# Kernel tuning notes

Measured on AMD Instinct MI355X. Metric: run time of the kernel, lower is better.

The kernel has to match this reference:

```python
import jax, jax.numpy as jnp
import numpy as np

B, N, C = 4, 2048, 768
H = 12
D = C // H  # head_dim = 64


def setup_inputs() -> dict:
    key = jax.random.key(0)
    k1, k2, k3, k4, k5 = jax.random.split(key, 5)
    s = 0.02
    return {
        "x": jax.random.normal(k1, (B, N, C), dtype=jnp.float32),
        "qkv_w": jax.random.normal(k2, (3 * C, C), dtype=jnp.float32) * s,
        "qkv_b": jax.random.normal(k3, (3 * C,), dtype=jnp.float32) * s,
        "proj_w": jax.random.normal(k4, (C, C), dtype=jnp.float32) * s,
        "proj_b": jax.random.normal(k5, (C,), dtype=jnp.float32) * s,
    }


def reference(x, qkv_w, qkv_b, proj_w, proj_b):
    b, n, c = x.shape
    # qkv projection (torch Linear: x @ W.T + b) -> [B,N,3,H,D] -> [3,B,H,N,D]
    qkv = (x @ qkv_w.T + qkv_b).reshape(b, n, 3, H, D).transpose(2, 0, 3, 1, 4)
    q, k, v = qkv[0], qkv[1], qkv[2]
    scale = D ** (-0.5)
    attn = jnp.einsum("bhqd,bhkd->bhqk", q, k) * scale
    attn = jax.nn.softmax(attn, axis=-1)
    # dropout is identity in eval mode
    out = jnp.einsum("bhqk,bhkd->bhqd", attn, v)  # [B,H,N,D]
    out = out.transpose(0, 2, 1, 3).reshape(b, n, c)
    return out @ proj_w.T + proj_b
```

## Files before the change

### kernel.cpp

```cpp
#include <hip/hip_runtime.h>
#include <hip/hip_bf16.h>
#include <stdint.h>

typedef __bf16 bf16_t;
typedef __bf16 bf16x8 __attribute__((ext_vector_type(8)));
typedef float f32x4 __attribute__((ext_vector_type(4)));

#define NB 4
#define NH 12
#define ND 64
#define NN 2048
#define NC 768

__device__ __forceinline__ void async_copy16(const bf16_t* g, bf16_t* l) {
    __builtin_amdgcn_global_load_lds((__attribute__((address_space(1))) void*)(void*)g,
                                     (__attribute__((address_space(3))) void*)l, 16, 0, 0);
}

__global__ void cast_kernel(const float* __restrict__ src, bf16_t* __restrict__ dst, int n4) {
    int i = blockIdx.x * blockDim.x + threadIdx.x;
    if (i >= n4) return;
    float4 v = ((const float4*)src)[i];
    union { bf16_t e[4]; uint2 u; } t;
    t.e[0] = (bf16_t)v.x; t.e[1] = (bf16_t)v.y; t.e[2] = (bf16_t)v.z; t.e[3] = (bf16_t)v.w;
    ((uint2*)dst)[i] = t.u;
}

__device__ __forceinline__ int vperm(int s) {
    return (s & 32) | (((s >> 2) & 3) << 3) | (((s >> 4) & 1) << 2) | (s & 3);
}


__launch_bounds__(256)
__global__ void qkv_gemm_kernel(const bf16_t* __restrict__ X, const bf16_t* __restrict__ W,
                                const float* __restrict__ bias,
                                bf16_t* __restrict__ Q, bf16_t* __restrict__ K, bf16_t* __restrict__ V)
{
    __shared__ __align__(16) bf16_t sA[128 * 64];
    __shared__ __align__(16) bf16_t sB[128 * 64];
    const int tid  = threadIdx.x;
    const int lane = tid & 63;
    const int w    = tid >> 6;
    const int wm   = w & 1, wn = w >> 1;
    const int m0   = blockIdx.x * 128;
    const int n0   = blockIdx.y * 128;
    const int lrow = lane & 15;
    const int quad = lane >> 4;
    const int arow = lane >> 3;
    const int gch  = (lane & 7) ^ arow;

    const int colbase = n0 + wn * 64;
    const int t3 = colbase / NC;
    const int h  = (colbase % NC) / ND;

    f32x4 zero = {0.f, 0.f, 0.f, 0.f};
    f32x4 acc[4][4];
#pragma unroll
    for (int i = 0; i < 4; ++i)
#pragma unroll
        for (int j = 0; j < 4; ++j) acc[i][j] = zero;

    for (int kt = 0; kt < NC; kt += 64) {
        __syncthreads();
        for (int c = w; c < 16; c += 4) {
            async_copy16(X + (size_t)(m0 + c * 8 + arow) * NC + kt + gch * 8, sA + c * 512);
            async_copy16(W + (size_t)(n0 + c * 8 + arow) * NC + kt + gch * 8, sB + c * 512);
        }
        __syncthreads();
#pragma unroll
        for (int hh = 0; hh < 2; ++hh) {
            bf16x8 xf[4], wf[4];
#pragma unroll
            for (int i = 0; i < 4; ++i) {
                int r = wm * 64 + i * 16 + lrow;
                xf[i] = *(const bf16x8*)(sA + r * 64 + (((hh * 4 + quad) ^ (r & 7)) * 8));
            }
#pragma unroll
            for (int j = 0; j < 4; ++j) {
                int r = wn * 64 + j * 16 + lrow;
                wf[j] = *(const bf16x8*)(sB + r * 64 + (((hh * 4 + quad) ^ (r & 7)) * 8));
            }
            if (t3 < 2) {
#pragma unroll
                for (int i = 0; i < 4; ++i)
#pragma unroll
                    for (int j = 0; j < 4; ++j)
                        acc[i][j] = __builtin_amdgcn_mfma_f32_16x16x32_bf16(wf[j], xf[i], acc[i][j], 0, 0, 0);
            } else {
#pragma unroll
                for (int i = 0; i < 4; ++i)
#pragma unroll
                    for (int j = 0; j < 4; ++j)
                        acc[i][j] = __builtin_amdgcn_mfma_f32_16x16x32_bf16(xf[i], wf[j], acc[i][j], 0, 0, 0);
            }
        }
    }

    const float qscale = 0.125f * 1.44269504088896340736f;

    if (t3 < 2) {
        bf16_t* outb = t3 ? K : Q;
#pragma unroll
        for (int j = 0; j < 4; ++j) {
            const int dcol = j * 16 + quad * 4;
            const float4 bv4 = *(const float4*)(bias + colbase + dcol);
#pragma unroll
            for (int i = 0; i < 4; ++i) {
                const int tok = m0 + wm * 64 + i * 16 + lrow;
                const int bb = tok >> 11;
                const int nn = tok & 2047;
                union { bf16_t e[4]; uint2 u; } pk;
#pragma unroll
                for (int p = 0; p < 4; ++p) {
                    float val = acc[i][j][p] + (&bv4.x)[p];
                    if (t3 == 0) val *= qscale;
                    pk.e[p] = (bf16_t)val;
                }
                *(uint2*)(outb + ((size_t)(bb * NH + h) * NN + nn) * ND + dcol) = pk.u;
            }
        }
    } else {
#pragma unroll
        for (int j = 0; j < 4; ++j) {
            const int d  = j * 16 + lrow;
            const float bv = bias[colbase + d];
#pragma unroll
            for (int i = 0; i < 4; ++i) {
                const int tok0 = m0 + wm * 64 + i * 16 + quad * 4;
                const int bb = tok0 >> 11;
                const int nn = tok0 & 2047;
                union { bf16_t e[4]; uint2 u; } pk;
#pragma unroll
                for (int p = 0; p < 4; ++p) pk.e[p] = (bf16_t)(acc[i][j][p] + bv);
                const int pos = (nn & ~63) | vperm(nn & 63);
                *(uint2*)(V + ((size_t)(bb * NH + h) * ND + d) * NN + pos) = pk.u;
            }
        }
    }
}

__launch_bounds__(512)
__global__ void attn_kernel(const bf16_t* __restrict__ Q, const bf16_t* __restrict__ K,
                            const bf16_t* __restrict__ Vt, bf16_t* __restrict__ O)
{
    __shared__ __align__(16) bf16_t sQ[128 * 64];
    __shared__ __align__(16) bf16_t sK[2][64 * 64];
    __shared__ __align__(16) bf16_t sV[2][64 * 64];
    const int tid  = threadIdx.x;
    const int lane = tid & 63;
    const int w    = tid >> 6;
    const int qt   = blockIdx.x;
    const int h    = blockIdx.y;
    const int b    = blockIdx.z;
    const int lrow = lane & 15;
    const int quad = lane >> 4;
    const int arow = lane >> 3;
    const int gch  = (lane & 7) ^ arow;
    const size_t head_off = (size_t)(b * NH + h) * NN * ND;
    const bf16_t* qh = Q  + head_off;
    const bf16_t* kh = K  + head_off;
    const bf16_t* vh = Vt + head_off;

    for (int c = w; c < 16; c += 8)
        async_copy16(qh + (size_t)(qt * 128 + c * 8 + arow) * ND + gch * 8, sQ + c * 512);
    __syncthreads();

    bf16x8 qb[2];
#pragma unroll
    for (int hh = 0; hh < 2; ++hh)
        qb[hh] = *(const bf16x8*)(sQ + (w * 16 + lrow) * 64 + (((hh * 4 + quad) ^ (lrow & 7)) * 8));

    f32x4 zero = {0.f, 0.f, 0.f, 0.f};
    f32x4 o[4];
#pragma unroll
    for (int db = 0; db < 4; ++db) o[db] = zero;
    float l_i = 0.f;

    const bf16_t* kbase = kh + (size_t)(w * 8 + arow) * ND + gch * 8;
    const bf16_t* vbase = vh + (size_t)(w * 8 + arow) * NN + gch * 8;

    for (int it = 0; it < NN / 128; ++it) {
        __syncthreads();
        async_copy16(kbase + (size_t)(it * 128) * ND,      sK[0] + w * 512);
        async_copy16(kbase + (size_t)(it * 128 + 64) * ND, sK[1] + w * 512);
        async_copy16(vbase + it * 128,                     sV[0] + w * 512);
        async_copy16(vbase + it * 128 + 64,                sV[1] + w * 512);
        __syncthreads();

#pragma unroll
        for (int half = 0; half < 2; ++half) {
            const bf16_t* sKh = sK[half];
            const bf16_t* sVh = sV[half];
            f32x4 s[4];
#pragma unroll
            for (int blk = 0; blk < 4; ++blk) {
                int r = blk * 16 + lrow;
                bf16x8 a0 = *(const bf16x8*)(sKh + r * 64 + ((quad ^ (r & 7)) * 8));
                bf16x8 a1 = *(const bf16x8*)(sKh + r * 64 + (((4 + quad) ^ (r & 7)) * 8));
                f32x4 z = zero;
                z = __builtin_amdgcn_mfma_f32_16x16x32_bf16(a0, qb[0], z, 0, 0, 0);
                z = __builtin_amdgcn_mfma_f32_16x16x32_bf16(a1, qb[1], z, 0, 0, 0);
                s[blk] = z;
            }

            union { __hip_bfloat162 h2[8]; bf16x8 v[2]; } pe;
            float rs0 = 0.f, rs1 = 0.f;
#pragma unroll
            for (int blk = 0; blk < 4; ++blk) {
                float e0 = exp2f(s[blk][0]);
                float e1 = exp2f(s[blk][1]);
                float e2 = exp2f(s[blk][2]);
                float e3 = exp2f(s[blk][3]);
                rs0 += e0 + e1;
                rs1 += e2 + e3;
                const int hb = (blk >> 1) * 4 + (blk & 1) * 2;
                pe.h2[hb]     = __float22bfloat162_rn(make_float2(e0, e1));
                pe.h2[hb + 1] = __float22bfloat162_rn(make_float2(e2, e3));
            }
            l_i += rs0 + rs1;

#pragma unroll
            for (int db = 0; db < 4; ++db) {
                int r = db * 16 + lrow;
                bf16x8 v0 = *(const bf16x8*)(sVh + r * 64 + ((quad ^ (r & 7)) * 8));
                bf16x8 v1 = *(const bf16x8*)(sVh + r * 64 + (((4 + quad) ^ (r & 7)) * 8));
                o[db] = __builtin_amdgcn_mfma_f32_16x16x32_bf16(v0, pe.v[0], o[db], 0, 0, 0);
                o[db] = __builtin_amdgcn_mfma_f32_16x16x32_bf16(v1, pe.v[1], o[db], 0, 0, 0);
            }
        }
    }

    l_i += __shfl_xor(l_i, 16);
    l_i += __shfl_xor(l_i, 32);
    const float rl = 1.0f / l_i;

    const int n = qt * 128 + w * 16 + lrow;
    const size_t rowoff = ((size_t)(b * NN + n)) * NC + h * ND;
#pragma unroll
    for (int db = 0; db < 4; ++db) {
        union { bf16_t e[4]; uint2 u; } pk;
#pragma unroll
        for (int p = 0; p < 4; ++p) pk.e[p] = (bf16_t)(o[db][p] * rl);
        *(uint2*)(O + rowoff + db * 16 + quad * 4) = pk.u;
    }
}

__launch_bounds__(256)
__global__ void proj_gemm_kernel(const bf16_t* __restrict__ A, const bf16_t* __restrict__ W,
                                 const float* __restrict__ bias, float* __restrict__ out)
{
    __shared__ __align__(16) bf16_t sA[128 * 64];
    __shared__ __align__(16) bf16_t sB[128 * 64];
    const int tid  = threadIdx.x;
    const int lane = tid & 63;
    const int w    = tid >> 6;
    const int wm   = w & 1, wn = w >> 1;
    const int m0   = blockIdx.x * 128;
    const int n0   = blockIdx.y * 128;
    const int lrow = lane & 15;
    const int quad = lane >> 4;
    const int arow = lane >> 3;
    const int gch  = (lane & 7) ^ arow;

    f32x4 zero = {0.f, 0.f, 0.f, 0.f};
    f32x4 acc[4][4];
#pragma unroll
    for (int i = 0; i < 4; ++i)
#pragma unroll
        for (int j = 0; j < 4; ++j) acc[i][j] = zero;

    for (int kt = 0; kt < NC; kt += 64) {
        __syncthreads();
        for (int c = w; c < 16; c += 4) {
            async_copy16(A + (size_t)(m0 + c * 8 + arow) * NC + kt + gch * 8, sA + c * 512);
            async_copy16(W + (size_t)(n0 + c * 8 + arow) * NC + kt + gch * 8, sB + c * 512);
        }
        __syncthreads();
#pragma unroll
        for (int hh = 0; hh < 2; ++hh) {
            bf16x8 xf[4], wf[4];
#pragma unroll
            for (int i = 0; i < 4; ++i) {
                int r = wm * 64 + i * 16 + lrow;
                xf[i] = *(const bf16x8*)(sA + r * 64 + (((hh * 4 + quad) ^ (r & 7)) * 8));
            }
#pragma unroll
            for (int j = 0; j < 4; ++j) {
                int r = wn * 64 + j * 16 + lrow;
                wf[j] = *(const bf16x8*)(sB + r * 64 + (((hh * 4 + quad) ^ (r & 7)) * 8));
            }
#pragma unroll
            for (int i = 0; i < 4; ++i)
#pragma unroll
                for (int j = 0; j < 4; ++j)
                    acc[i][j] = __builtin_amdgcn_mfma_f32_16x16x32_bf16(wf[j], xf[i], acc[i][j], 0, 0, 0);
        }
    }

#pragma unroll
    for (int j = 0; j < 4; ++j) {
        const int colg0 = n0 + wn * 64 + j * 16 + quad * 4;
        const float4 bv4 = *(const float4*)(bias + colg0);
#pragma unroll
        for (int i = 0; i < 4; ++i) {
            const int tok = m0 + wm * 64 + i * 16 + lrow;
            float4 val;
#pragma unroll
            for (int p = 0; p < 4; ++p) (&val.x)[p] = acc[i][j][p] + (&bv4.x)[p];
            *(float4*)(out + (size_t)tok * NC + colg0) = val;
        }
    }
}

extern "C" void kernel_launch(void* const* d_in, const int* in_sizes, int n_in,
                              void* d_out, int out_size, void* d_ws, size_t ws_size,
                              hipStream_t stream) {
    const float* x      = (const float*)d_in[0];
    const float* qkv_w  = (const float*)d_in[1];
    const float* qkv_b  = (const float*)d_in[2];
    const float* proj_w = (const float*)d_in[3];
    const float* proj_b = (const float*)d_in[4];
    float* out = (float*)d_out;

    char* ws = (char*)d_ws;
    bf16_t* xb    = (bf16_t*)ws; ws += (size_t)8192 * 768 * 2;
    bf16_t* wqkv  = (bf16_t*)ws; ws += (size_t)2304 * 768 * 2;
    bf16_t* wproj = (bf16_t*)ws; ws += (size_t)768 * 768 * 2;
    bf16_t* qb    = (bf16_t*)ws; ws += (size_t)NB * NH * NN * ND * 2;
    bf16_t* kb    = (bf16_t*)ws; ws += (size_t)NB * NH * NN * ND * 2;
    bf16_t* vb    = (bf16_t*)ws; ws += (size_t)NB * NH * NN * ND * 2;
    bf16_t* ab    = (bf16_t*)ws; ws += (size_t)8192 * 768 * 2;

    cast_kernel<<<(8192 * 768 / 4 + 255) / 256, 256, 0, stream>>>(x, xb, 8192 * 768 / 4);
    cast_kernel<<<(2304 * 768 / 4 + 255) / 256, 256, 0, stream>>>(qkv_w, wqkv, 2304 * 768 / 4);
    cast_kernel<<<(768 * 768 / 4 + 255) / 256, 256, 0, stream>>>(proj_w, wproj, 768 * 768 / 4);

    qkv_gemm_kernel<<<dim3(8192 / 128, 2304 / 128), 256, 0, stream>>>(xb, wqkv, qkv_b, qb, kb, vb);
    attn_kernel<<<dim3(NN / 128, NH, NB), 512, 0, stream>>>(qb, kb, vb, ab);
    proj_gemm_kernel<<<dim3(8192 / 128, 768 / 128), 256, 0, stream>>>(ab, wproj, proj_b, out);
}
```

Measured before the change: 234.9 us.

## Give each attention wave two query tiles, shrink blocks, split QKV GEMM by V

The attention kernel now runs 256 threads per block, and each wave handles 32 query rows (two 16-row tiles). Each K/V fragment read from LDS therefore feeds twice as many MFMAs. The Q, K and V buffers share one LDS array, and swizzle offsets are precomputed. The QKV GEMM is split into two template launches (Q/K and V) to remove a runtime branch around the MFMA loop. The trade-off is higher register pressure from the doubled accumulators, plus an extra kernel launch.

```diff
diff --git a/kernel.cpp b/kernel.cpp
--- a/kernel.cpp
+++ b/kernel.cpp
@@ -5,6 +5,7 @@
 typedef __bf16 bf16_t;
 typedef __bf16 bf16x8 __attribute__((ext_vector_type(8)));
 typedef float f32x4 __attribute__((ext_vector_type(4)));
+typedef unsigned int u32x4 __attribute__((ext_vector_type(4)));
 
 #define NB 4
 #define NH 12
@@ -15,6 +16,13 @@
 __device__ __forceinline__ void async_copy16(const bf16_t* g, bf16_t* l) {
     __builtin_amdgcn_global_load_lds((__attribute__((address_space(1))) void*)(void*)g,
                                      (__attribute__((address_space(3))) void*)l, 16, 0, 0);
+}
+
+__device__ __forceinline__ unsigned pack_bf2(float a, float b) {
+    union { bf16_t e[2]; unsigned u; } t;
+    t.e[0] = (bf16_t)a;
+    t.e[1] = (bf16_t)b;
+    return t.u;
 }
 
 __global__ void cast_kernel(const float* __restrict__ src, bf16_t* __restrict__ dst, int n4) {
@@ -31,10 +39,12 @@
 }
 
 
+template <bool ISV>
 __launch_bounds__(256)
 __global__ void qkv_gemm_kernel(const bf16_t* __restrict__ X, const bf16_t* __restrict__ W,
                                 const float* __restrict__ bias,
-                                bf16_t* __restrict__ Q, bf16_t* __restrict__ K, bf16_t* __restrict__ V)
+                                bf16_t* __restrict__ Q, bf16_t* __restrict__ K, bf16_t* __restrict__ V,
+                                int n0base)
 {
     __shared__ __align__(16) bf16_t sA[128 * 64];
     __shared__ __align__(16) bf16_t sB[128 * 64];
@@ -43,15 +53,13 @@
     const int w    = tid >> 6;
     const int wm   = w & 1, wn = w >> 1;
     const int m0   = blockIdx.x * 128;
-    const int n0   = blockIdx.y * 128;
+    const int n0   = n0base + blockIdx.y * 128;
     const int lrow = lane & 15;
     const int quad = lane >> 4;
     const int arow = lane >> 3;
     const int gch  = (lane & 7) ^ arow;
 
     const int colbase = n0 + wn * 64;
-    const int t3 = colbase / NC;
-    const int h  = (colbase % NC) / ND;
 
     f32x4 zero = {0.f, 0.f, 0.f, 0.f};
     f32x4 acc[4][4];
@@ -80,25 +88,23 @@
                 int r = wn * 64 + j * 16 + lrow;
                 wf[j] = *(const bf16x8*)(sB + r * 64 + (((hh * 4 + quad) ^ (r & 7)) * 8));
             }
-            if (t3 < 2) {
-#pragma unroll
-                for (int i = 0; i < 4; ++i)
-#pragma unroll
-                    for (int j = 0; j < 4; ++j)
+#pragma unroll
+            for (int i = 0; i < 4; ++i)
+#pragma unroll
+                for (int j = 0; j < 4; ++j) {
+                    if (ISV)
+                        acc[i][j] = __builtin_amdgcn_mfma_f32_16x16x32_bf16(xf[i], wf[j], acc[i][j], 0, 0, 0);
+                    else
                         acc[i][j] = __builtin_amdgcn_mfma_f32_16x16x32_bf16(wf[j], xf[i], acc[i][j], 0, 0, 0);
-            } else {
-#pragma unroll
-                for (int i = 0; i < 4; ++i)
-#pragma unroll
-                    for (int j = 0; j < 4; ++j)
-                        acc[i][j] = __builtin_amdgcn_mfma_f32_16x16x32_bf16(xf[i], wf[j], acc[i][j], 0, 0, 0);
-            }
+                }
         }
     }
 
     const float qscale = 0.125f * 1.44269504088896340736f;
 
-    if (t3 < 2) {
+    if (!ISV) {
+        const int t3 = colbase / NC;
+        const int h  = (colbase % NC) / ND;
         bf16_t* outb = t3 ? K : Q;
 #pragma unroll
         for (int j = 0; j < 4; ++j) {
@@ -120,6 +126,7 @@
             }
         }
     } else {
+        const int h = (colbase - 2 * NC) / ND;
 #pragma unroll
         for (int j = 0; j < 4; ++j) {
             const int d  = j * 16 + lrow;
@@ -139,13 +146,12 @@
     }
 }
 
-__launch_bounds__(512)
+__launch_bounds__(256, 4)
 __global__ void attn_kernel(const bf16_t* __restrict__ Q, const bf16_t* __restrict__ K,
                             const bf16_t* __restrict__ Vt, bf16_t* __restrict__ O)
 {
-    __shared__ __align__(16) bf16_t sQ[128 * 64];
-    __shared__ __align__(16) bf16_t sK[2][64 * 64];
-    __shared__ __align__(16) bf16_t sV[2][64 * 64];
+    __shared__ __align__(16) bf16_t sKV[4][64 * 64];
+    bf16_t* sQ = sKV[0];
     const int tid  = threadIdx.x;
     const int lane = tid & 63;
     const int w    = tid >> 6;
@@ -161,87 +167,125 @@
     const bf16_t* kh = K  + head_off;
     const bf16_t* vh = Vt + head_off;
 
-    for (int c = w; c < 16; c += 8)
-        async_copy16(qh + (size_t)(qt * 128 + c * 8 + arow) * ND + gch * 8, sQ + c * 512);
+#pragma unroll
+    for (int c = 0; c < 4; ++c)
+        async_copy16(qh + (size_t)(qt * 128 + (w * 4 + c) * 8 + arow) * ND + gch * 8,
+                     sQ + (w * 4 + c) * 512);
     __syncthreads();
 
-    bf16x8 qb[2];
-#pragma unroll
-    for (int hh = 0; hh < 2; ++hh)
-        qb[hh] = *(const bf16x8*)(sQ + (w * 16 + lrow) * 64 + (((hh * 4 + quad) ^ (lrow & 7)) * 8));
+    bf16x8 qb[2][2];
+#pragma unroll
+    for (int qi = 0; qi < 2; ++qi)
+#pragma unroll
+        for (int hh = 0; hh < 2; ++hh) {
+            int r = w * 32 + qi * 16 + lrow;
+            qb[qi][hh] = *(const bf16x8*)(sQ + r * 64 + (((hh * 4 + quad) ^ (r & 7)) * 8));
+        }
+
+    int off[4][2];
+#pragma unroll
+    for (int blk = 0; blk < 4; ++blk) {
+        int r = blk * 16 + lrow;
+        off[blk][0] = r * 64 + ((quad ^ (r & 7)) * 8);
+        off[blk][1] = r * 64 + (((4 + quad) ^ (r & 7)) * 8);
+    }
 
     f32x4 zero = {0.f, 0.f, 0.f, 0.f};
-    f32x4 o[4];
-#pragma unroll
-    for (int db = 0; db < 4; ++db) o[db] = zero;
-    float l_i = 0.f;
-
-    const bf16_t* kbase = kh + (size_t)(w * 8 + arow) * ND + gch * 8;
-    const bf16_t* vbase = vh + (size_t)(w * 8 + arow) * NN + gch * 8;
+    f32x4 o[2][4];
+#pragma unroll
+    for (int qi = 0; qi < 2; ++qi)
+#pragma unroll
+        for (int db = 0; db < 4; ++db) o[qi][db] = zero;
+    float l_i[2] = {0.f, 0.f};
+
+    const bf16_t* kp = kh + (size_t)(w * 16 + arow) * ND + gch * 8;
+    const bf16_t* vp = vh + (size_t)(w * 16 + arow) * NN + gch * 8;
 
     for (int it = 0; it < NN / 128; ++it) {
         __syncthreads();
-        async_copy16(kbase + (size_t)(it * 128) * ND,      sK[0] + w * 512);
-        async_copy16(kbase + (size_t)(it * 128 + 64) * ND, sK[1] + w * 512);
-        async_copy16(vbase + it * 128,                     sV[0] + w * 512);
-        async_copy16(vbase + it * 128 + 64,                sV[1] + w * 512);
-        __syncthreads();
+        async_copy16(kp,               sKV[0] + w * 1024);
+        async_copy16(kp + 8 * ND,      sKV[0] + w * 1024 + 512);
+        async_copy16(kp + 64 * ND,     sKV[1] + w * 1024);
+        async_copy16(kp + 72 * ND,     sKV[1] + w * 1024 + 512);
+        async_copy16(vp,               sKV[2] + w * 1024);
+        async_copy16(vp + 8 * NN,      sKV[2] + w * 1024 + 512);
+        async_copy16(vp + 64,          sKV[3] + w * 1024);
+        async_copy16(vp + 8 * NN + 64, sKV[3] + w * 1024 + 512);
+        __syncthreads();
+        kp += 128 * ND;
+        vp += 128;
 
 #pragma unroll
         for (int half = 0; half < 2; ++half) {
-            const bf16_t* sKh = sK[half];
-            const bf16_t* sVh = sV[half];
-            f32x4 s[4];
+            const bf16_t* sKh = sKV[half];
+            const bf16_t* sVh = sKV[2 + half];
+
+            f32x4 s[2][4];
 #pragma unroll
             for (int blk = 0; blk < 4; ++blk) {
-                int r = blk * 16 + lrow;
-                bf16x8 a0 = *(const bf16x8*)(sKh + r * 64 + ((quad ^ (r & 7)) * 8));
-                bf16x8 a1 = *(const bf16x8*)(sKh + r * 64 + (((4 + quad) ^ (r & 7)) * 8));
-                f32x4 z = zero;
-                z = __builtin_amdgcn_mfma_f32_16x16x32_bf16(a0, qb[0], z, 0, 0, 0);
-                z = __builtin_amdgcn_mfma_f32_16x16x32_bf16(a1, qb[1], z, 0, 0, 0);
-                s[blk] = z;
-            }
-
-            union { __hip_bfloat162 h2[8]; bf16x8 v[2]; } pe;
-            float rs0 = 0.f, rs1 = 0.f;
-#pragma unroll
-            for (int blk = 0; blk < 4; ++blk) {
-                float e0 = exp2f(s[blk][0]);
-                float e1 = exp2f(s[blk][1]);
-                float e2 = exp2f(s[blk][2]);
-                float e3 = exp2f(s[blk][3]);
-                rs0 += e0 + e1;
-                rs1 += e2 + e3;
-                const int hb = (blk >> 1) * 4 + (blk & 1) * 2;
-                pe.h2[hb]     = __float22bfloat162_rn(make_float2(e0, e1));
-                pe.h2[hb + 1] = __float22bfloat162_rn(make_float2(e2, e3));
-            }
-            l_i += rs0 + rs1;
+                bf16x8 a0 = *(const bf16x8*)(sKh + off[blk][0]);
+                bf16x8 a1 = *(const bf16x8*)(sKh + off[blk][1]);
+#pragma unroll
+                for (int qi = 0; qi < 2; ++qi) {
+                    f32x4 z = zero;
+                    z = __builtin_amdgcn_mfma_f32_16x16x32_bf16(a0, qb[qi][0], z, 0, 0, 0);
+                    z = __builtin_amdgcn_mfma_f32_16x16x32_bf16(a1, qb[qi][1], z, 0, 0, 0);
+                    s[qi][blk] = z;
+                }
+            }
+
+            bf16x8 pe[2][2];
+#pragma unroll
+            for (int qi = 0; qi < 2; ++qi) {
+                u32x4 pu0 = {0, 0, 0, 0}, pu1 = {0, 0, 0, 0};
+                float r0 = 0.f, r1 = 0.f;
+#pragma unroll
+                for (int blk = 0; blk < 4; ++blk) {
+                    float e0 = __builtin_amdgcn_exp2f(s[qi][blk][0]);
+                    float e1 = __builtin_amdgcn_exp2f(s[qi][blk][1]);
+                    float e2 = __builtin_amdgcn_exp2f(s[qi][blk][2]);
+                    float e3 = __builtin_amdgcn_exp2f(s[qi][blk][3]);
+                    r0 += e0 + e1;
+                    r1 += e2 + e3;
+                    unsigned lo = pack_bf2(e0, e1), hi = pack_bf2(e2, e3);
+                    if (blk == 0)      { pu0[0] = lo; pu0[1] = hi; }
+                    else if (blk == 1) { pu0[2] = lo; pu0[3] = hi; }
+                    else if (blk == 2) { pu1[0] = lo; pu1[1] = hi; }
+                    else               { pu1[2] = lo; pu1[3] = hi; }
+                }
+                pe[qi][0] = __builtin_bit_cast(bf16x8, pu0);
+                pe[qi][1] = __builtin_bit_cast(bf16x8, pu1);
+                l_i[qi] += r0 + r1;
+            }
 
 #pragma unroll
             for (int db = 0; db < 4; ++db) {
-                int r = db * 16 + lrow;
-                bf16x8 v0 = *(const bf16x8*)(sVh + r * 64 + ((quad ^ (r & 7)) * 8));
-                bf16x8 v1 = *(const bf16x8*)(sVh + r * 64 + (((4 + quad) ^ (r & 7)) * 8));
-                o[db] = __builtin_amdgcn_mfma_f32_16x16x32_bf16(v0, pe.v[0], o[db], 0, 0, 0);
-                o[db] = __builtin_amdgcn_mfma_f32_16x16x32_bf16(v1, pe.v[1], o[db], 0, 0, 0);
-            }
-        }
-    }
-
-    l_i += __shfl_xor(l_i, 16);
-    l_i += __shfl_xor(l_i, 32);
-    const float rl = 1.0f / l_i;
-
-    const int n = qt * 128 + w * 16 + lrow;
-    const size_t rowoff = ((size_t)(b * NN + n)) * NC + h * ND;
-#pragma unroll
-    for (int db = 0; db < 4; ++db) {
-        union { bf16_t e[4]; uint2 u; } pk;
-#pragma unroll
-        for (int p = 0; p < 4; ++p) pk.e[p] = (bf16_t)(o[db][p] * rl);
-        *(uint2*)(O + rowoff + db * 16 + quad * 4) = pk.u;
+                bf16x8 v0 = *(const bf16x8*)(sVh + off[db][0]);
+                bf16x8 v1 = *(const bf16x8*)(sVh + off[db][1]);
+#pragma unroll
+                for (int qi = 0; qi < 2; ++qi) {
+                    o[qi][db] = __builtin_amdgcn_mfma_f32_16x16x32_bf16(v0, pe[qi][0], o[qi][db], 0, 0, 0);
+                    o[qi][db] = __builtin_amdgcn_mfma_f32_16x16x32_bf16(v1, pe[qi][1], o[qi][db], 0, 0, 0);
+                }
+            }
+        }
+    }
+
+#pragma unroll
+    for (int qi = 0; qi < 2; ++qi) {
+        float l = l_i[qi];
+        l += __shfl_xor(l, 16);
+        l += __shfl_xor(l, 32);
+        const float rl = 1.0f / l;
+        const int n = qt * 128 + w * 32 + qi * 16 + lrow;
+        const size_t rowoff = ((size_t)(b * NN + n)) * NC + h * ND;
+#pragma unroll
+        for (int db = 0; db < 4; ++db) {
+            union { bf16_t e[4]; uint2 u; } pk;
+#pragma unroll
+            for (int p = 0; p < 4; ++p) pk.e[p] = (bf16_t)(o[qi][db][p] * rl);
+            *(uint2*)(O + rowoff + db * 16 + quad * 4) = pk.u;
+        }
     }
 }
 
@@ -335,7 +379,8 @@
     cast_kernel<<<(2304 * 768 / 4 + 255) / 256, 256, 0, stream>>>(qkv_w, wqkv, 2304 * 768 / 4);
     cast_kernel<<<(768 * 768 / 4 + 255) / 256, 256, 0, stream>>>(proj_w, wproj, 768 * 768 / 4);
 
-    qkv_gemm_kernel<<<dim3(8192 / 128, 2304 / 128), 256, 0, stream>>>(xb, wqkv, qkv_b, qb, kb, vb);
-    attn_kernel<<<dim3(NN / 128, NH, NB), 512, 0, stream>>>(qb, kb, vb, ab);
+    qkv_gemm_kernel<false><<<dim3(8192 / 128, 12), 256, 0, stream>>>(xb, wqkv, qkv_b, qb, kb, vb, 0);
+    qkv_gemm_kernel<true><<<dim3(8192 / 128, 6), 256, 0, stream>>>(xb, wqkv, qkv_b, qb, kb, vb, 1536);
+    attn_kernel<<<dim3(NN / 128, NH, NB), 256, 0, stream>>>(qb, kb, vb, ab);
     proj_gemm_kernel<<<dim3(8192 / 128, 768 / 128), 256, 0, stream>>>(ab, wproj, proj_b, out);
 }
```

New measurement: 238.7 us. No clear change (+1.6%).
